# Kernel optimization log

Measured on AMD Instinct MI355X. Metric: run time of the kernel, lower is better.

Reference implementation:

```python
import jax, jax.numpy as jnp
import numpy as np

B, c, H, W = 64, 3, 512, 512
R = 8  # region_num
C = B * c

def setup_inputs() -> dict:
    key = jax.random.key(0)
    k1, k2, k3 = jax.random.split(key, 3)
    return {
        "x": jax.random.normal(k1, (B, c, H, W), dtype=jnp.float32),
        "region_percentiles": jax.random.uniform(k2, (C * (R - 1),), dtype=jnp.float32),
        "proxy_percentiles": jax.random.uniform(k3, (C * R,), dtype=jnp.float32),
        "region_num": R,
    }

def reference(x, region_percentiles, proxy_percentiles, region_num):
    Bx, cx, Hx, Wx = x.shape
    Cx = Bx * cx
    xf = x.reshape(Cx, Hx * Wx)                       # (C, HW)
    min_val = xf.min(axis=1)                          # (C,)
    max_val = xf.max(axis=1)                          # (C,)
    # random percentile boundary positions per channel, sorted
    pos = (region_percentiles.reshape(Cx, region_num - 1)
           * (max_val - min_val)[:, None] + min_val[:, None])
    pos_sorted = jnp.sort(pos, axis=1)                # (C, R-1)
    # region ends: left = [min, pos...], right = [pos..., max + 1e-6]
    left = jnp.concatenate([min_val[:, None], pos_sorted], axis=1)          # (C, R)
    right = jnp.concatenate([pos_sorted, max_val[:, None] + 1e-6], axis=1)  # (C, R)
    # region id for each pixel: number of boundaries <= x (== argmax of inside-mask)
    ids = jax.vmap(lambda bnd, v: jnp.searchsorted(bnd, v, side='right'))(pos_sorted, xf)  # (C, HW) int32
    # random value inside each region, then gather per pixel
    rand_vals = left + proxy_percentiles.reshape(Cx, region_num) * (right - left)  # (C, R)
    proxy = jnp.take_along_axis(rand_vals, ids, axis=1)                            # (C, HW)
    return proxy.reshape(Bx, cx, Hx, Wx).astype(x.dtype)
```

## Files before the change

### kernel.cpp

```cpp
#include <hip/hip_runtime.h>
#include <math.h>

#pragma clang fp contract(off)

#define CCH   192
#define HW    (512*512)
#define RNUM  8
#define SUB   4
#define X4_PER_CH (HW / 4)
#define SLAB  (X4_PER_CH / SUB)
#define PT    (SLAB / 256)
#define NREG  16
#define NLDS  9
#define NUNH  (PT - NREG - NLDS)

typedef float f32x4 __attribute__((ext_vector_type(4)));

__device__ __forceinline__ float mul_rn(float a, float b) {
    float r; asm volatile("v_mul_f32 %0, %1, %2" : "=v"(r) : "v"(a), "v"(b)); return r;
}
__device__ __forceinline__ float add_rn(float a, float b) {
    float r; asm volatile("v_add_f32 %0, %1, %2" : "=v"(r) : "v"(a), "v"(b)); return r;
}
__device__ __forceinline__ float sub_rn(float a, float b) {
    float r; asm volatile("v_sub_f32 %0, %1, %2" : "=v"(r) : "v"(a), "v"(b)); return r;
}

__device__ __forceinline__ float bst_sel(float v,
    float b0, float b1, float b2, float b3, float b4, float b5, float b6,
    float r0, float r1, float r2, float r3, float r4, float r5, float r6, float r7) {
    return (v < b3) ? ((v < b1) ? ((v < b0) ? r0 : r1)
                                : ((v < b2) ? r2 : r3))
                    : ((v < b5) ? ((v < b4) ? r4 : r5)
                                : ((v < b6) ? r6 : r7));
}

__global__ __launch_bounds__(256, 4) void k_fused(
        const float* __restrict__ xg,
        const float* __restrict__ region_percentiles,
        const float* __restrict__ proxy_percentiles,
        float* __restrict__ outg,
        int*   __restrict__ cnt,
        float* __restrict__ part) {
    const int tid  = threadIdx.x;
    const int chan = blockIdx.x / SUB;
    const int sub  = blockIdx.x % SUB;

    const f32x4* px = (const f32x4*)xg + (size_t)chan * X4_PER_CH + (size_t)sub * SLAB;
    f32x4*       po = (f32x4*)outg     + (size_t)chan * X4_PER_CH + (size_t)sub * SLAB;

    __shared__ f32x4 slds[NLDS * 256];
    __shared__ float smn[256], smx[256];
    __shared__ float sprm[16];

    float hx[NREG], hy[NREG], hz[NREG], hw[NREG];
    float mn = INFINITY, mx = -INFINITY;
    #pragma unroll
    for (int k = 0; k < NREG; ++k) {
        const f32x4 t = px[k * 256 + tid];
        hx[k] = t.x; hy[k] = t.y; hz[k] = t.z; hw[k] = t.w;
        mn = fminf(mn, fminf(fminf(t.x, t.y), fminf(t.z, t.w)));
        mx = fmaxf(mx, fmaxf(fmaxf(t.x, t.y), fmaxf(t.z, t.w)));
    }
    #pragma unroll
    for (int k = 0; k < NREG; ++k)
        asm volatile("" : "+v"(hx[k]), "+v"(hy[k]), "+v"(hz[k]), "+v"(hw[k]));

    #pragma unroll
    for (int j = 0; j < NLDS; ++j) {
        const f32x4 t = px[(NREG + j) * 256 + tid];
        mn = fminf(mn, fminf(fminf(t.x, t.y), fminf(t.z, t.w)));
        mx = fmaxf(mx, fmaxf(fmaxf(t.x, t.y), fmaxf(t.z, t.w)));
        slds[j * 256 + tid] = t;
    }
    #pragma unroll 8
    for (int j = 0; j < NUNH; ++j) {
        const f32x4 t = px[(NREG + NLDS + j) * 256 + tid];
        mn = fminf(mn, fminf(fminf(t.x, t.y), fminf(t.z, t.w)));
        mx = fmaxf(mx, fmaxf(fmaxf(t.x, t.y), fmaxf(t.z, t.w)));
    }

    smn[tid] = mn; smx[tid] = mx;
    __syncthreads();
    for (int s = 128; s > 0; s >>= 1) {
        if (tid < s) {
            smn[tid] = fminf(smn[tid], smn[tid + s]);
            smx[tid] = fmaxf(smx[tid], smx[tid + s]);
        }
        __syncthreads();
    }

    if (tid == 0) {
        __hip_atomic_store(&part[chan * 16 + sub * 2 + 0], smn[0],
                           __ATOMIC_RELAXED, __HIP_MEMORY_SCOPE_AGENT);
        __hip_atomic_store(&part[chan * 16 + sub * 2 + 1], smx[0],
                           __ATOMIC_RELAXED, __HIP_MEMORY_SCOPE_AGENT);
        __hip_atomic_fetch_add(&cnt[chan], 1,
                               __ATOMIC_RELEASE, __HIP_MEMORY_SCOPE_AGENT);
        while (__hip_atomic_load(&cnt[chan], __ATOMIC_RELAXED,
                                 __HIP_MEMORY_SCOPE_AGENT) < SUB)
            __builtin_amdgcn_s_sleep(8);
        __builtin_amdgcn_fence(__ATOMIC_ACQUIRE, "agent");

        float cmn = INFINITY, cmx = -INFINITY;
        #pragma unroll
        for (int p = 0; p < SUB; ++p) {
            cmn = fminf(cmn, __hip_atomic_load(&part[chan * 16 + p * 2 + 0],
                              __ATOMIC_RELAXED, __HIP_MEMORY_SCOPE_AGENT));
            cmx = fmaxf(cmx, __hip_atomic_load(&part[chan * 16 + p * 2 + 1],
                              __ATOMIC_RELAXED, __HIP_MEMORY_SCOPE_AGENT));
        }
        const float range = sub_rn(cmx, cmn);

        float pos[RNUM - 1];
        #pragma unroll
        for (int i = 0; i < RNUM - 1; ++i)
            pos[i] = add_rn(mul_rn(region_percentiles[chan * (RNUM - 1) + i], range), cmn);
        for (int i = 1; i < RNUM - 1; ++i) {
            float v = pos[i];
            int j = i - 1;
            while (j >= 0 && pos[j] > v) { pos[j + 1] = pos[j]; --j; }
            pos[j + 1] = v;
        }
        #pragma unroll
        for (int i = 0; i < RNUM - 1; ++i) sprm[i] = pos[i];
        #pragma unroll
        for (int i = 0; i < RNUM; ++i) {
            const float left  = (i == 0)        ? cmn : pos[i - 1];
            const float right = (i == RNUM - 1) ? add_rn(cmx, 1e-6f) : pos[i];
            sprm[RNUM - 1 + i] = add_rn(left,
                                        mul_rn(proxy_percentiles[chan * RNUM + i],
                                               sub_rn(right, left)));
        }
    }
    __syncthreads();

    const float b0 = sprm[0], b1 = sprm[1], b2 = sprm[2], b3 = sprm[3];
    const float b4 = sprm[4], b5 = sprm[5], b6 = sprm[6];
    const float r0 = sprm[7],  r1 = sprm[8],  r2 = sprm[9],  r3 = sprm[10];
    const float r4 = sprm[11], r5 = sprm[12], r6 = sprm[13], r7 = sprm[14];

    #pragma unroll 8
    for (int j = 0; j < NUNH; ++j) {
        const int idx = (NREG + NLDS + j) * 256 + tid;
        const f32x4 v = px[idx];
        f32x4 o;
        o.x = bst_sel(v.x, b0,b1,b2,b3,b4,b5,b6, r0,r1,r2,r3,r4,r5,r6,r7);
        o.y = bst_sel(v.y, b0,b1,b2,b3,b4,b5,b6, r0,r1,r2,r3,r4,r5,r6,r7);
        o.z = bst_sel(v.z, b0,b1,b2,b3,b4,b5,b6, r0,r1,r2,r3,r4,r5,r6,r7);
        o.w = bst_sel(v.w, b0,b1,b2,b3,b4,b5,b6, r0,r1,r2,r3,r4,r5,r6,r7);
        __builtin_nontemporal_store(o, &po[idx]);
    }
    #pragma unroll
    for (int j = 0; j < NLDS; ++j) {
        const f32x4 v = slds[j * 256 + tid];
        f32x4 o;
        o.x = bst_sel(v.x, b0,b1,b2,b3,b4,b5,b6, r0,r1,r2,r3,r4,r5,r6,r7);
        o.y = bst_sel(v.y, b0,b1,b2,b3,b4,b5,b6, r0,r1,r2,r3,r4,r5,r6,r7);
        o.z = bst_sel(v.z, b0,b1,b2,b3,b4,b5,b6, r0,r1,r2,r3,r4,r5,r6,r7);
        o.w = bst_sel(v.w, b0,b1,b2,b3,b4,b5,b6, r0,r1,r2,r3,r4,r5,r6,r7);
        __builtin_nontemporal_store(o, &po[(NREG + j) * 256 + tid]);
    }
    #pragma unroll
    for (int k = 0; k < NREG; ++k) {
        f32x4 o;
        o.x = bst_sel(hx[k], b0,b1,b2,b3,b4,b5,b6, r0,r1,r2,r3,r4,r5,r6,r7);
        o.y = bst_sel(hy[k], b0,b1,b2,b3,b4,b5,b6, r0,r1,r2,r3,r4,r5,r6,r7);
        o.z = bst_sel(hz[k], b0,b1,b2,b3,b4,b5,b6, r0,r1,r2,r3,r4,r5,r6,r7);
        o.w = bst_sel(hw[k], b0,b1,b2,b3,b4,b5,b6, r0,r1,r2,r3,r4,r5,r6,r7);
        __builtin_nontemporal_store(o, &po[k * 256 + tid]);
    }
}

extern "C" void kernel_launch(void* const* d_in, const int* in_sizes, int n_in,
                              void* d_out, int out_size, void* d_ws, size_t ws_size,
                              hipStream_t stream) {
    const float* x  = (const float*)d_in[0];
    const float* rp = (const float*)d_in[1];
    const float* pp = (const float*)d_in[2];
    float* out = (float*)d_out;

    int*   cnt  = (int*)d_ws;
    float* part = (float*)((char*)d_ws + 1024);

    (void)hipMemsetAsync(d_ws, 0, 1024, stream);

    k_fused<<<CCH * SUB, 256, 0, stream>>>(x, rp, pp, out, cnt, part);
}
```

Before: 114.7 us.

## Use one 512-thread block per channel and drop inter-block atomic sync

Each channel is now handled by a single 512-thread block instead of four cooperating 256-thread blocks. This removes the atomic partial-min/max exchange, the spin-wait and the workspace memset. The share of each channel held in registers and LDS grows, so less of the input is read a second time from global memory. In exchange, the grid shrinks to 192 blocks, fewer than the CU count. The much larger register and LDS footprint per thread also risks spills and limits occupancy.

```diff
diff --git a/kernel.cpp b/kernel.cpp
--- a/kernel.cpp
+++ b/kernel.cpp
@@ -6,12 +6,11 @@
 #define CCH   192
 #define HW    (512*512)
 #define RNUM  8
-#define SUB   4
+#define THREADS 512
 #define X4_PER_CH (HW / 4)
-#define SLAB  (X4_PER_CH / SUB)
-#define PT    (SLAB / 256)
-#define NREG  16
-#define NLDS  9
+#define PT    (X4_PER_CH / THREADS)
+#define NREG  48
+#define NLDS  14
 #define NUNH  (PT - NREG - NLDS)
 
 typedef float f32x4 __attribute__((ext_vector_type(4)));
@@ -35,29 +34,26 @@
                                 : ((v < b6) ? r6 : r7));
 }
 
-__global__ __launch_bounds__(256, 4) void k_fused(
+__global__ __launch_bounds__(THREADS, 2) void k_fused(
         const float* __restrict__ xg,
         const float* __restrict__ region_percentiles,
         const float* __restrict__ proxy_percentiles,
-        float* __restrict__ outg,
-        int*   __restrict__ cnt,
-        float* __restrict__ part) {
+        float* __restrict__ outg) {
     const int tid  = threadIdx.x;
-    const int chan = blockIdx.x / SUB;
-    const int sub  = blockIdx.x % SUB;
+    const int chan = blockIdx.x;
 
-    const f32x4* px = (const f32x4*)xg + (size_t)chan * X4_PER_CH + (size_t)sub * SLAB;
-    f32x4*       po = (f32x4*)outg     + (size_t)chan * X4_PER_CH + (size_t)sub * SLAB;
+    const f32x4* px = (const f32x4*)xg + (size_t)chan * X4_PER_CH;
+    f32x4*       po = (f32x4*)outg     + (size_t)chan * X4_PER_CH;
 
-    __shared__ f32x4 slds[NLDS * 256];
-    __shared__ float smn[256], smx[256];
+    __shared__ f32x4 slds[NLDS * THREADS];
+    __shared__ float smn[THREADS], smx[THREADS];
     __shared__ float sprm[16];
 
     float hx[NREG], hy[NREG], hz[NREG], hw[NREG];
     float mn = INFINITY, mx = -INFINITY;
     #pragma unroll
     for (int k = 0; k < NREG; ++k) {
-        const f32x4 t = px[k * 256 + tid];
+        const f32x4 t = px[k * THREADS + tid];
         hx[k] = t.x; hy[k] = t.y; hz[k] = t.z; hw[k] = t.w;
         mn = fminf(mn, fminf(fminf(t.x, t.y), fminf(t.z, t.w)));
         mx = fmaxf(mx, fmaxf(fmaxf(t.x, t.y), fmaxf(t.z, t.w)));
@@ -68,21 +64,21 @@
 
     #pragma unroll
     for (int j = 0; j < NLDS; ++j) {
-        const f32x4 t = px[(NREG + j) * 256 + tid];
+        const f32x4 t = px[(NREG + j) * THREADS + tid];
         mn = fminf(mn, fminf(fminf(t.x, t.y), fminf(t.z, t.w)));
         mx = fmaxf(mx, fmaxf(fmaxf(t.x, t.y), fmaxf(t.z, t.w)));
-        slds[j * 256 + tid] = t;
+        slds[j * THREADS + tid] = t;
     }
     #pragma unroll 8
     for (int j = 0; j < NUNH; ++j) {
-        const f32x4 t = px[(NREG + NLDS + j) * 256 + tid];
+        const f32x4 t = px[(NREG + NLDS + j) * THREADS + tid];
         mn = fminf(mn, fminf(fminf(t.x, t.y), fminf(t.z, t.w)));
         mx = fmaxf(mx, fmaxf(fmaxf(t.x, t.y), fmaxf(t.z, t.w)));
     }
 
     smn[tid] = mn; smx[tid] = mx;
     __syncthreads();
-    for (int s = 128; s > 0; s >>= 1) {
+    for (int s = THREADS / 2; s > 0; s >>= 1) {
         if (tid < s) {
             smn[tid] = fminf(smn[tid], smn[tid + s]);
             smx[tid] = fmaxf(smx[tid], smx[tid + s]);
@@ -91,25 +87,8 @@
     }
 
     if (tid == 0) {
-        __hip_atomic_store(&part[chan * 16 + sub * 2 + 0], smn[0],
-                           __ATOMIC_RELAXED, __HIP_MEMORY_SCOPE_AGENT);
-        __hip_atomic_store(&part[chan * 16 + sub * 2 + 1], smx[0],
-                           __ATOMIC_RELAXED, __HIP_MEMORY_SCOPE_AGENT);
-        __hip_atomic_fetch_add(&cnt[chan], 1,
-                               __ATOMIC_RELEASE, __HIP_MEMORY_SCOPE_AGENT);
-        while (__hip_atomic_load(&cnt[chan], __ATOMIC_RELAXED,
-                                 __HIP_MEMORY_SCOPE_AGENT) < SUB)
-            __builtin_amdgcn_s_sleep(8);
-        __builtin_amdgcn_fence(__ATOMIC_ACQUIRE, "agent");
-
-        float cmn = INFINITY, cmx = -INFINITY;
-        #pragma unroll
-        for (int p = 0; p < SUB; ++p) {
-            cmn = fminf(cmn, __hip_atomic_load(&part[chan * 16 + p * 2 + 0],
-                              __ATOMIC_RELAXED, __HIP_MEMORY_SCOPE_AGENT));
-            cmx = fmaxf(cmx, __hip_atomic_load(&part[chan * 16 + p * 2 + 1],
-                              __ATOMIC_RELAXED, __HIP_MEMORY_SCOPE_AGENT));
-        }
+        const float cmn = smn[0];
+        const float cmx = smx[0];
         const float range = sub_rn(cmx, cmn);
 
         float pos[RNUM - 1];
@@ -142,7 +121,7 @@
 
     #pragma unroll 8
     for (int j = 0; j < NUNH; ++j) {
-        const int idx = (NREG + NLDS + j) * 256 + tid;
+        const int idx = (NREG + NLDS + j) * THREADS + tid;
         const f32x4 v = px[idx];
         f32x4 o;
         o.x = bst_sel(v.x, b0,b1,b2,b3,b4,b5,b6, r0,r1,r2,r3,r4,r5,r6,r7);
@@ -153,13 +132,13 @@
     }
     #pragma unroll
     for (int j = 0; j < NLDS; ++j) {
-        const f32x4 v = slds[j * 256 + tid];
+        const f32x4 v = slds[j * THREADS + tid];
         f32x4 o;
         o.x = bst_sel(v.x, b0,b1,b2,b3,b4,b5,b6, r0,r1,r2,r3,r4,r5,r6,r7);
         o.y = bst_sel(v.y, b0,b1,b2,b3,b4,b5,b6, r0,r1,r2,r3,r4,r5,r6,r7);
         o.z = bst_sel(v.z, b0,b1,b2,b3,b4,b5,b6, r0,r1,r2,r3,r4,r5,r6,r7);
         o.w = bst_sel(v.w, b0,b1,b2,b3,b4,b5,b6, r0,r1,r2,r3,r4,r5,r6,r7);
-        __builtin_nontemporal_store(o, &po[(NREG + j) * 256 + tid]);
+        __builtin_nontemporal_store(o, &po[(NREG + j) * THREADS + tid]);
     }
     #pragma unroll
     for (int k = 0; k < NREG; ++k) {
@@ -168,7 +147,7 @@
         o.y = bst_sel(hy[k], b0,b1,b2,b3,b4,b5,b6, r0,r1,r2,r3,r4,r5,r6,r7);
         o.z = bst_sel(hz[k], b0,b1,b2,b3,b4,b5,b6, r0,r1,r2,r3,r4,r5,r6,r7);
         o.w = bst_sel(hw[k], b0,b1,b2,b3,b4,b5,b6, r0,r1,r2,r3,r4,r5,r6,r7);
-        __builtin_nontemporal_store(o, &po[k * 256 + tid]);
+        __builtin_nontemporal_store(o, &po[k * THREADS + tid]);
     }
 }
 
@@ -180,10 +159,5 @@
     const float* pp = (const float*)d_in[2];
     float* out = (float*)d_out;
 
-    int*   cnt  = (int*)d_ws;
-    float* part = (float*)((char*)d_ws + 1024);
-
-    (void)hipMemsetAsync(d_ws, 0, 1024, stream);
-
-    k_fused<<<CCH * SUB, 256, 0, stream>>>(x, rp, pp, out, cnt, part);
+    k_fused<<<CCH, THREADS, 0, stream>>>(x, rp, pp, out);
 }
```

After: 134.0 us. +16.8%, slower.
